# Kernel tuning notes

Measured on AMD Instinct MI355X. Metric: run time of the kernel, lower is better.

Reference implementation:

```python
import jax, jax.numpy as jnp
import numpy as np

REG = 0.1  # config['reg']


def _poly_filter(s, gammas):
    # Horner evaluation of sum_k gammas[k] * s**k (monomial basis, depth K=len-1).
    out = jnp.full_like(s, gammas[-1])
    for k in range(gammas.shape[0] - 2, -1, -1):
        out = out * s + gammas[k]
    return out


def setup_inputs() -> dict:
    key = jax.random.key(0)
    k1, k2, k3, k4, k5 = jax.random.split(key, 5)
    B, H, N, R = 4, 8, 4096, 64
    U = jax.random.normal(k1, (B, H, N, R), dtype=jnp.float32)
    Sigma = jax.random.normal(k2, (B, H, 1, R), dtype=jnp.float32)
    svd_V = jax.random.normal(k3, (B, H, N, R), dtype=jnp.float32)
    V = jax.random.normal(k4, (B, H, N, R), dtype=jnp.float32)
    mask = jnp.ones((B, N), dtype=jnp.float32)
    # learnable polynomial coefficients; gamma_0 fixed to 1 (fixI=True)
    gammas = jnp.concatenate([jnp.ones((1,), jnp.float32),
                              0.1 * jax.random.normal(k5, (4,), dtype=jnp.float32)])
    return {"U": U, "Sigma": Sigma, "svd_V": svd_V, "V": V, "mask": mask, "gammas": gammas}


def reference(U, Sigma, svd_V, V, mask, gammas):
    # Q: softmax over rank dim r
    Q = jax.nn.softmax(U, axis=-1)                                      # [B,H,N,r]
    # K: masked softmax over sequence dim N
    Kmat = jax.nn.softmax(svd_V - 1e9 * (1.0 - mask[:, None, :, None]), axis=-2)
    S = jax.nn.sigmoid(Sigma)                                           # [B,H,1,r]
    graph_filter = _poly_filter(S, gammas)                              # [B,H,1,r]
    # linear-attention ordering: (Q*filt) @ (K^T @ V), never forms NxN
    KtV = jnp.einsum('bhnr,bhnd->bhrd', Kmat, V)                        # [B,H,r,d]
    X = jnp.einsum('bhnr,bhrd->bhnd', Q * graph_filter, KtV)            # [B,H,N,d]
    r = Q.shape[-1]
    eye = jnp.eye(r, dtype=Q.dtype)
    symQ = jnp.einsum('bhnr,bhns->bhrs', Q, Q) - eye
    ortho_loss = REG * jnp.mean(jnp.abs(symQ), axis=(1, 2, 3))
    symK = jnp.einsum('bhnr,bhns->bhrs', Kmat, Kmat) - eye
    ortho_loss = ortho_loss + REG * jnp.mean(jnp.abs(symK), axis=(1, 2, 3))
    return X, ortho_loss
```

## Files before the change

### kernel.cpp

```cpp
#include <hip/hip_runtime.h>
#include <math.h>

#define NB 4
#define NH 8
#define BHN 32
#define SN 4096
#define RR 64
#define REGC 0.1f

#define MCH 16
#define MROWS 256
#define XCH 32
#define XROWS 128

typedef short s16x8 __attribute__((ext_vector_type(8)));
typedef float f32x4 __attribute__((ext_vector_type(4)));

__device__ __forceinline__ float wave_sum(float v) {
    #pragma unroll
    for (int off = 32; off; off >>= 1) v += __shfl_xor(v, off, 64);
    return v;
}
__device__ __forceinline__ float wave_sum64(float v) {
    v += __int_as_float(__builtin_amdgcn_update_dpp(0, __float_as_int(v), 0x121, 0xf, 0xf, true));
    v += __int_as_float(__builtin_amdgcn_update_dpp(0, __float_as_int(v), 0x122, 0xf, 0xf, true));
    v += __int_as_float(__builtin_amdgcn_update_dpp(0, __float_as_int(v), 0x124, 0xf, 0xf, true));
    v += __int_as_float(__builtin_amdgcn_update_dpp(0, __float_as_int(v), 0x128, 0xf, 0xf, true));
    v += __shfl_xor(v, 16, 64);
    v += __shfl_xor(v, 32, 64);
    return v;
}
__device__ __forceinline__ float octet_sum(float v) {
    v += __int_as_float(__builtin_amdgcn_update_dpp(0, __float_as_int(v), 0xB1, 0xf, 0xf, true));
    v += __int_as_float(__builtin_amdgcn_update_dpp(0, __float_as_int(v), 0x4E, 0xf, 0xf, true));
    v += __shfl_xor(v, 4, 64);
    return v;
}
__device__ __forceinline__ unsigned short f2bf(float x) {
    unsigned int u = __float_as_uint(x);
    u += 0x7FFFu + ((u >> 16) & 1u);
    return (unsigned short)(u >> 16);
}
__device__ __forceinline__ float bf2f(unsigned short h) {
    return __uint_as_float(((unsigned int)h) << 16);
}
__device__ __forceinline__ unsigned int packbf(float a, float b) {
    return (unsigned int)f2bf(a) | ((unsigned int)f2bf(b) << 16);
}
__device__ __forceinline__ s16x8 ldfrag(const unsigned int* p) {
    uint4 r = *(const uint4*)p;
    return __builtin_bit_cast(s16x8, r);
}
__device__ __forceinline__ int swz(int row, int blk) {
    return (row << 5) + (((blk ^ (row & 7))) << 2);
}
__device__ __forceinline__ uint4 pack8(const float* x) {
    return make_uint4(packbf(x[0], x[1]), packbf(x[2], x[3]),
                      packbf(x[4], x[5]), packbf(x[6], x[7]));
}

__global__ void k_zero_loss(float* loss) {
    if (threadIdx.x < NB) loss[threadIdx.x] = 0.0f;
}

#define PH 0
#define VH 2048
#define QH 4096
__launch_bounds__(512, 4)
__global__ void k_main(const float* __restrict__ U, const float* __restrict__ sv,
                       const float* __restrict__ V, const float* __restrict__ mask,
                       float* __restrict__ ktv_part, float* __restrict__ symk_part,
                       float* __restrict__ symq_part, float* __restrict__ colsum_part) {
    __shared__ __align__(16) unsigned int sm[12288];
    const int chunk = blockIdx.x, bh = blockIdx.y, b = bh >> 3;
    const int t = threadIdx.x, l = t & 63, w = t >> 6;
    const int r15 = l & 15, quad = l >> 4;
    const int ni = w & 3, mi0 = (w >> 2) << 1;
    const size_t rowbase = (size_t)bh * SN * RR;
    const int row0 = chunk * MROWS;

    float csum = 0.0f;
    f32x4 aKV[2], aSK[2], aSQ[2];
    #pragma unroll
    for (int j = 0; j < 2; j++) {
        aKV[j] = (f32x4){0.f, 0.f, 0.f, 0.f};
        aSK[j] = (f32x4){0.f, 0.f, 0.f, 0.f};
        aSQ[j] = (f32x4){0.f, 0.f, 0.f, 0.f};
    }

    float bu[2][8], bx[2][8], bv[2][8];
    #pragma unroll
    for (int i = 0; i < 8; i++) {
        const size_t off = rowbase + (size_t)(row0 + 8 * w + i) * RR + l;
        bu[0][i] = U[off]; bx[0][i] = sv[off]; bv[0][i] = V[off];
    }

    #pragma unroll
    for (int s = 0; s < 4; s++) {
        const int cur = s & 1, nxt = cur ^ 1;
        const int nb = row0 + s * 64;
        const int bufb = cur * 6144;
        float bm[8];
        #pragma unroll
        for (int i = 0; i < 8; i++) bm[i] = mask[b * SN + nb + 8 * w + i];
        float q[8], p[8];
        #pragma unroll
        for (int i = 0; i < 8; i++) {
            const float eu = __expf(bu[cur][i]);
            q[i] = eu * (1.0f / wave_sum64(eu));
        }
        #pragma unroll
        for (int i = 0; i < 8; i++) {
            p[i] = __expf(bx[cur][i] - 1e9f * (1.0f - bm[i]));
            csum += p[i];
        }
        if (s < 3) {
            #pragma unroll
            for (int i = 0; i < 8; i++) {
                const size_t off = rowbase + (size_t)(nb + 64 + 8 * w + i) * RR + l;
                bu[nxt][i] = U[off]; bx[nxt][i] = sv[off]; bv[nxt][i] = V[off];
            }
        }
        const uint4 ph = pack8(p);
        const uint4 vh = pack8(bv[cur]);
        const uint4 qh = pack8(q);
        const int wbase = bufb + (l << 5) + ((w ^ (l & 7)) << 2);
        *(uint4*)(sm + PH + wbase) = ph;
        *(uint4*)(sm + VH + wbase) = vh;
        *(uint4*)(sm + QH + wbase) = qh;
        __syncthreads();
        #pragma unroll
        for (int ks = 0; ks < 2; ks++) {
            const int ub = ks * 4 + quad;
            s16x8 Ah[2], AQ[2];
            #pragma unroll
            for (int j = 0; j < 2; j++) {
                const int oa = bufb + swz((mi0 + j) * 16 + r15, ub);
                Ah[j] = ldfrag(sm + PH + oa);
                AQ[j] = ldfrag(sm + QH + oa);
            }
            const int ob = bufb + swz(ni * 16 + r15, ub);
            const s16x8 Bvh = ldfrag(sm + VH + ob);
            const s16x8 Bph = ldfrag(sm + PH + ob);
            const s16x8 Bq  = ldfrag(sm + QH + ob);
            #pragma unroll
            for (int j = 0; j < 2; j++) {
                aKV[j] = __builtin_amdgcn_mfma_f32_16x16x32_bf16(Ah[j], Bvh, aKV[j], 0, 0, 0);
                aSK[j] = __builtin_amdgcn_mfma_f32_16x16x32_bf16(Ah[j], Bph, aSK[j], 0, 0, 0);
                aSQ[j] = __builtin_amdgcn_mfma_f32_16x16x32_bf16(AQ[j], Bq,  aSQ[j], 0, 0, 0);
            }
        }
    }
    const size_t pb = ((size_t)bh * MCH + chunk) * 4096;
    #pragma unroll
    for (int j = 0; j < 2; j++)
        #pragma unroll
        for (int r = 0; r < 4; r++) {
            const int e = ((mi0 + j) * 16 + quad * 4 + r) * 64 + ni * 16 + r15;
            ktv_part[pb + e]  = aKV[j][r];
            symk_part[pb + e] = aSK[j][r];
            symq_part[pb + e] = aSQ[j][r];
        }
    __syncthreads();
    float* smf = (float*)sm;
    smf[w * 64 + l] = csum;
    __syncthreads();
    if (w == 0) {
        float scol = 0.f;
        #pragma unroll
        for (int j = 0; j < 8; j++) scol += smf[j * 64 + l];
        colsum_part[(bh * MCH + chunk) * 64 + l] = scol;
    }
}

__global__ void k_finalize(const float* __restrict__ ktv_part, const float* __restrict__ symk_part,
                           const float* __restrict__ symq_part, const float* __restrict__ colsum_part,
                           const float* __restrict__ Sigma, const float* __restrict__ gammas,
                           unsigned short* __restrict__ ktvt_hi, unsigned short* __restrict__ ktvt_lo,
                           float* __restrict__ loss) {
    const int rb = blockIdx.x, bh = blockIdx.y, b = bh >> 3, t = threadIdx.x;
    __shared__ float cs[64];
    if (t < 64) {
        float s = 0.f;
        for (int c = 0; c < MCH; c++) s += colsum_part[(bh * MCH + c) * 64 + t];
        cs[t] = s;
    }
    __syncthreads();
    const float g0 = gammas[0], g1 = gammas[1], g2 = gammas[2], g3 = gammas[3], g4 = gammas[4];
    float lsum = 0.0f;
    #pragma unroll
    for (int o = 0; o < 2; o++) {
        const int idx = rb * 512 + o * 256 + t;
        const int r = idx >> 6, c = idx & 63;
        float kv = 0.f, sk = 0.f, sq = 0.f;
        for (int ch = 0; ch < MCH; ch++) {
            const size_t pb = ((size_t)bh * MCH + ch) * 4096 + idx;
            kv += ktv_part[pb]; sk += symk_part[pb]; sq += symq_part[pb];
        }
        const float iSr = 1.0f / cs[r], iSc = 1.0f / cs[c];
        kv *= iSr;
        sk *= iSr * iSc;
        const float sg = 1.0f / (1.0f + __expf(-Sigma[bh * 64 + r]));
        float f = g4; f = f * sg + g3; f = f * sg + g2; f = f * sg + g1; f = f * sg + g0;
        const float kvf = kv * f;
        const unsigned short h = f2bf(kvf);
        ktvt_hi[bh * 4096 + c * 64 + r] = h;
        ktvt_lo[bh * 4096 + c * 64 + r] = f2bf(kvf - bf2f(h));
        const float eye = (r == c) ? 1.0f : 0.0f;
        lsum += fabsf(sk - eye) + fabsf(sq - eye);
    }
    lsum = wave_sum(lsum);
    __shared__ float smr[4];
    if ((t & 63) == 0) smr[t >> 6] = lsum;
    __syncthreads();
    if (t == 0)
        atomicAdd(loss + b, (REGC / (NH * 64.0f * 64.0f)) * (smr[0] + smr[1] + smr[2] + smr[3]));
}

__launch_bounds__(512, 8)
__global__ void k_xq(const float* __restrict__ U,
                     const unsigned short* __restrict__ ktvt_hi,
                     const unsigned short* __restrict__ ktvt_lo,
                     float* __restrict__ Xout) {
    __shared__ __align__(16) unsigned int sm[4096];
    const int chunk = blockIdx.x, bh = blockIdx.y;
    const int t = threadIdx.x, l = t & 63, w = t >> 6;
    const int r15 = l & 15, quad = l >> 4;
    const int ni = w & 3, mi0 = (w >> 2) << 1;
    const size_t rowbase = (size_t)bh * SN * RR;
    const int row0 = chunk * XROWS;
    const int nl = 8 * w + (l >> 3);
    const int c0 = (l & 7) * 8;

    s16x8 Bh[2], Bl[2];
    #pragma unroll
    for (int ks = 0; ks < 2; ks++) {
        const int idx = (ni * 16 + r15) * 64 + ks * 32 + quad * 8;
        Bh[ks] = __builtin_bit_cast(s16x8, *(const uint4*)(ktvt_hi + (size_t)bh * 4096 + idx));
        Bl[ks] = __builtin_bit_cast(s16x8, *(const uint4*)(ktvt_lo + (size_t)bh * 4096 + idx));
    }

    float4 ba[2], bb[2];
    {
        const float* src = U + rowbase + (size_t)(row0 + nl) * RR + c0;
        ba[0] = *(const float4*)src;
        bb[0] = *(const float4*)(src + 4);
    }

    #pragma unroll
    for (int s = 0; s < 2; s++) {
        const int cur = s & 1, nxt = cur ^ 1;
        const int nb = row0 + s * 64;
        const int bufb = cur * 2048;
        float e[8];
        e[0] = __expf(ba[cur].x); e[1] = __expf(ba[cur].y);
        e[2] = __expf(ba[cur].z); e[3] = __expf(ba[cur].w);
        e[4] = __expf(bb[cur].x); e[5] = __expf(bb[cur].y);
        e[6] = __expf(bb[cur].z); e[7] = __expf(bb[cur].w);
        float loc = 0.f;
        #pragma unroll
        for (int i = 0; i < 8; i++) loc += e[i];
        const float inv = 1.0f / octet_sum(loc);
        if (s < 1) {
            const float* src = U + rowbase + (size_t)(nb + 64 + nl) * RR + c0;
            ba[nxt] = *(const float4*)src;
            bb[nxt] = *(const float4*)(src + 4);
        }
        float q[8];
        #pragma unroll
        for (int i = 0; i < 8; i++) q[i] = e[i] * inv;
        *(uint4*)(sm + bufb + swz(nl, l & 7)) = pack8(q);
        __syncthreads();
        f32x4 acc[2];
        acc[0] = (f32x4){0.f, 0.f, 0.f, 0.f};
        acc[1] = (f32x4){0.f, 0.f, 0.f, 0.f};
        #pragma unroll
        for (int ks = 0; ks < 2; ks++) {
            #pragma unroll
            for (int jj = 0; jj < 2; jj++) {
                const int oa = bufb + swz((mi0 + jj) * 16 + r15, ks * 4 + quad);
                const s16x8 Ah = ldfrag(sm + oa);
                acc[jj] = __builtin_amdgcn_mfma_f32_16x16x32_bf16(Ah, Bh[ks], acc[jj], 0, 0, 0);
                acc[jj] = __builtin_amdgcn_mfma_f32_16x16x32_bf16(Ah, Bl[ks], acc[jj], 0, 0, 0);
            }
        }
        #pragma unroll
        for (int jj = 0; jj < 2; jj++)
            #pragma unroll
            for (int r = 0; r < 4; r++) {
                const int n = nb + (mi0 + jj) * 16 + quad * 4 + r;
                Xout[rowbase + (size_t)n * RR + ni * 16 + r15] = acc[jj][r];
            }
    }
}

extern "C" void kernel_launch(void* const* d_in, const int* in_sizes, int n_in,
                              void* d_out, int out_size, void* d_ws, size_t ws_size,
                              hipStream_t stream) {
    (void)in_sizes; (void)n_in; (void)out_size; (void)ws_size;
    const float* U      = (const float*)d_in[0];
    const float* Sigma  = (const float*)d_in[1];
    const float* sv     = (const float*)d_in[2];
    const float* V      = (const float*)d_in[3];
    const float* mask   = (const float*)d_in[4];
    const float* gammas = (const float*)d_in[5];

    float* X    = (float*)d_out;
    float* loss = X + (size_t)BHN * SN * RR;

    float* ws          = (float*)d_ws;
    float* ktv_part    = ws;
    float* symk_part   = ktv_part + (size_t)BHN * MCH * 4096;
    float* symq_part   = symk_part + (size_t)BHN * MCH * 4096;
    float* colsum_part = symq_part + (size_t)BHN * MCH * 4096;
    unsigned short* ktvt_hi = (unsigned short*)(colsum_part + BHN * MCH * 64);
    unsigned short* ktvt_lo = ktvt_hi + BHN * 4096;

    hipLaunchKernelGGL(k_zero_loss, dim3(1), dim3(64), 0, stream, loss);
    hipLaunchKernelGGL(k_main, dim3(MCH, BHN), dim3(512), 0, stream,
                       U, sv, V, mask, ktv_part, symk_part, symq_part, colsum_part);
    hipLaunchKernelGGL(k_finalize, dim3(8, BHN), dim3(256), 0, stream,
                       ktv_part, symk_part, symq_part, colsum_part, Sigma, gammas,
                       ktvt_hi, ktvt_lo, loss);
    hipLaunchKernelGGL(k_xq, dim3(XCH, BHN), dim3(512), 0, stream,
                       U, ktvt_hi, ktvt_lo, X);
}
```

Before: 157.7 us.

## Split main pass into more chunks, drop loss-zero kernel, vectorize finalize

Doubles the number of chunks in the main reduction kernel (128 rows each, single LDS buffer, higher occupancy bound) to give more blocks in flight. Removes the separate loss-zeroing launch and atomics by writing per-block loss partials and reducing them inside the X kernel. Vectorizes the finalize partial-sum reads with float2, uses a raw hardware reciprocal instead of division, and moves prefetch loads earlier. This doubles the partial-buffer traffic read in finalize and relies on the approximate rcp for accuracy.

```diff
diff --git a/kernel.cpp b/kernel.cpp
--- a/kernel.cpp
+++ b/kernel.cpp
@@ -8,8 +8,8 @@
 #define RR 64
 #define REGC 0.1f
 
-#define MCH 16
-#define MROWS 256
+#define MCH 32
+#define MROWS 128
 #define XCH 32
 #define XROWS 128
 
@@ -36,6 +36,9 @@
     v += __shfl_xor(v, 4, 64);
     return v;
 }
+__device__ __forceinline__ float fastrcp(float x) {
+    float r; asm("v_rcp_f32 %0, %1" : "=v"(r) : "v"(x)); return r;
+}
 __device__ __forceinline__ unsigned short f2bf(float x) {
     unsigned int u = __float_as_uint(x);
     u += 0x7FFFu + ((u >> 16) & 1u);
@@ -59,19 +62,15 @@
                       packbf(x[4], x[5]), packbf(x[6], x[7]));
 }
 
-__global__ void k_zero_loss(float* loss) {
-    if (threadIdx.x < NB) loss[threadIdx.x] = 0.0f;
-}
-
 #define PH 0
 #define VH 2048
 #define QH 4096
-__launch_bounds__(512, 4)
+__launch_bounds__(512, 8)
 __global__ void k_main(const float* __restrict__ U, const float* __restrict__ sv,
                        const float* __restrict__ V, const float* __restrict__ mask,
                        float* __restrict__ ktv_part, float* __restrict__ symk_part,
                        float* __restrict__ symq_part, float* __restrict__ colsum_part) {
-    __shared__ __align__(16) unsigned int sm[12288];
+    __shared__ __align__(16) unsigned int sm[6144];
     const int chunk = blockIdx.x, bh = blockIdx.y, b = bh >> 3;
     const int t = threadIdx.x, l = t & 63, w = t >> 6;
     const int r15 = l & 15, quad = l >> 4;
@@ -96,10 +95,16 @@
     }
 
     #pragma unroll
-    for (int s = 0; s < 4; s++) {
+    for (int s = 0; s < 2; s++) {
         const int cur = s & 1, nxt = cur ^ 1;
         const int nb = row0 + s * 64;
-        const int bufb = cur * 6144;
+        if (s < 1) {
+            #pragma unroll
+            for (int i = 0; i < 8; i++) {
+                const size_t off = rowbase + (size_t)(nb + 64 + 8 * w + i) * RR + l;
+                bu[nxt][i] = U[off]; bx[nxt][i] = sv[off]; bv[nxt][i] = V[off];
+            }
+        }
         float bm[8];
         #pragma unroll
         for (int i = 0; i < 8; i++) bm[i] = mask[b * SN + nb + 8 * w + i];
@@ -107,24 +112,18 @@
         #pragma unroll
         for (int i = 0; i < 8; i++) {
             const float eu = __expf(bu[cur][i]);
-            q[i] = eu * (1.0f / wave_sum64(eu));
+            q[i] = eu * fastrcp(wave_sum64(eu));
         }
         #pragma unroll
         for (int i = 0; i < 8; i++) {
             p[i] = __expf(bx[cur][i] - 1e9f * (1.0f - bm[i]));
             csum += p[i];
         }
-        if (s < 3) {
-            #pragma unroll
-            for (int i = 0; i < 8; i++) {
-                const size_t off = rowbase + (size_t)(nb + 64 + 8 * w + i) * RR + l;
-                bu[nxt][i] = U[off]; bx[nxt][i] = sv[off]; bv[nxt][i] = V[off];
-            }
-        }
         const uint4 ph = pack8(p);
         const uint4 vh = pack8(bv[cur]);
         const uint4 qh = pack8(q);
-        const int wbase = bufb + (l << 5) + ((w ^ (l & 7)) << 2);
+        const int wbase = (l << 5) + ((w ^ (l & 7)) << 2);
+        if (s > 0) __syncthreads();
         *(uint4*)(sm + PH + wbase) = ph;
         *(uint4*)(sm + VH + wbase) = vh;
         *(uint4*)(sm + QH + wbase) = qh;
@@ -135,11 +134,11 @@
             s16x8 Ah[2], AQ[2];
             #pragma unroll
             for (int j = 0; j < 2; j++) {
-                const int oa = bufb + swz((mi0 + j) * 16 + r15, ub);
+                const int oa = swz((mi0 + j) * 16 + r15, ub);
                 Ah[j] = ldfrag(sm + PH + oa);
                 AQ[j] = ldfrag(sm + QH + oa);
             }
-            const int ob = bufb + swz(ni * 16 + r15, ub);
+            const int ob = swz(ni * 16 + r15, ub);
             const s16x8 Bvh = ldfrag(sm + VH + ob);
             const s16x8 Bph = ldfrag(sm + PH + ob);
             const s16x8 Bq  = ldfrag(sm + QH + ob);
@@ -177,8 +176,8 @@
                            const float* __restrict__ symq_part, const float* __restrict__ colsum_part,
                            const float* __restrict__ Sigma, const float* __restrict__ gammas,
                            unsigned short* __restrict__ ktvt_hi, unsigned short* __restrict__ ktvt_lo,
-                           float* __restrict__ loss) {
-    const int rb = blockIdx.x, bh = blockIdx.y, b = bh >> 3, t = threadIdx.x;
+                           float* __restrict__ loss_part) {
+    const int rb = blockIdx.x, bh = blockIdx.y, t = threadIdx.x;
     __shared__ float cs[64];
     if (t < 64) {
         float s = 0.f;
@@ -187,41 +186,45 @@
     }
     __syncthreads();
     const float g0 = gammas[0], g1 = gammas[1], g2 = gammas[2], g3 = gammas[3], g4 = gammas[4];
-    float lsum = 0.0f;
-    #pragma unroll
-    for (int o = 0; o < 2; o++) {
-        const int idx = rb * 512 + o * 256 + t;
-        const int r = idx >> 6, c = idx & 63;
-        float kv = 0.f, sk = 0.f, sq = 0.f;
-        for (int ch = 0; ch < MCH; ch++) {
-            const size_t pb = ((size_t)bh * MCH + ch) * 4096 + idx;
-            kv += ktv_part[pb]; sk += symk_part[pb]; sq += symq_part[pb];
-        }
-        const float iSr = 1.0f / cs[r], iSc = 1.0f / cs[c];
-        kv *= iSr;
-        sk *= iSr * iSc;
-        const float sg = 1.0f / (1.0f + __expf(-Sigma[bh * 64 + r]));
-        float f = g4; f = f * sg + g3; f = f * sg + g2; f = f * sg + g1; f = f * sg + g0;
-        const float kvf = kv * f;
-        const unsigned short h = f2bf(kvf);
-        ktvt_hi[bh * 4096 + c * 64 + r] = h;
-        ktvt_lo[bh * 4096 + c * 64 + r] = f2bf(kvf - bf2f(h));
-        const float eye = (r == c) ? 1.0f : 0.0f;
-        lsum += fabsf(sk - eye) + fabsf(sq - eye);
-    }
+    const int idx = rb * 512 + t * 2;
+    const int r = idx >> 6, c = idx & 63;
+    float2 kv = make_float2(0.f, 0.f), sk = make_float2(0.f, 0.f), sq = make_float2(0.f, 0.f);
+    #pragma unroll 4
+    for (int ch = 0; ch < MCH; ch++) {
+        const size_t pb = ((size_t)bh * MCH + ch) * 4096 + idx;
+        const float2 a = *(const float2*)(ktv_part + pb);
+        const float2 bq = *(const float2*)(symk_part + pb);
+        const float2 cq = *(const float2*)(symq_part + pb);
+        kv.x += a.x;  kv.y += a.y;
+        sk.x += bq.x; sk.y += bq.y;
+        sq.x += cq.x; sq.y += cq.y;
+    }
+    const float iSr = fastrcp(cs[r]);
+    const float iSc0 = fastrcp(cs[c]), iSc1 = fastrcp(cs[c + 1]);
+    const float sg = fastrcp(1.0f + __expf(-Sigma[bh * 64 + r]));
+    float f = g4; f = f * sg + g3; f = f * sg + g2; f = f * sg + g1; f = f * sg + g0;
+    const float kvf0 = kv.x * iSr * f, kvf1 = kv.y * iSr * f;
+    const unsigned short h0 = f2bf(kvf0), h1 = f2bf(kvf1);
+    ktvt_hi[bh * 4096 + c * 64 + r] = h0;
+    ktvt_lo[bh * 4096 + c * 64 + r] = f2bf(kvf0 - bf2f(h0));
+    ktvt_hi[bh * 4096 + (c + 1) * 64 + r] = h1;
+    ktvt_lo[bh * 4096 + (c + 1) * 64 + r] = f2bf(kvf1 - bf2f(h1));
+    const float eye0 = (r == c) ? 1.0f : 0.0f, eye1 = (r == c + 1) ? 1.0f : 0.0f;
+    float lsum = fabsf(sk.x * iSr * iSc0 - eye0) + fabsf(sk.y * iSr * iSc1 - eye1)
+               + fabsf(sq.x - eye0) + fabsf(sq.y - eye1);
     lsum = wave_sum(lsum);
     __shared__ float smr[4];
     if ((t & 63) == 0) smr[t >> 6] = lsum;
     __syncthreads();
-    if (t == 0)
-        atomicAdd(loss + b, (REGC / (NH * 64.0f * 64.0f)) * (smr[0] + smr[1] + smr[2] + smr[3]));
+    if (t == 0) loss_part[bh * 8 + rb] = smr[0] + smr[1] + smr[2] + smr[3];
 }
 
 __launch_bounds__(512, 8)
 __global__ void k_xq(const float* __restrict__ U,
                      const unsigned short* __restrict__ ktvt_hi,
                      const unsigned short* __restrict__ ktvt_lo,
-                     float* __restrict__ Xout) {
+                     const float* __restrict__ loss_part,
+                     float* __restrict__ Xout, float* __restrict__ loss) {
     __shared__ __align__(16) unsigned int sm[4096];
     const int chunk = blockIdx.x, bh = blockIdx.y;
     const int t = threadIdx.x, l = t & 63, w = t >> 6;
@@ -232,6 +235,11 @@
     const int nl = 8 * w + (l >> 3);
     const int c0 = (l & 7) * 8;
 
+    if (chunk == 0 && bh == 0 && t < 256) {
+        const float v = wave_sum(loss_part[t]);
+        if ((t & 63) == 0) loss[t >> 6] = (REGC / (NH * 64.0f * 64.0f)) * v;
+    }
+
     s16x8 Bh[2], Bl[2];
     #pragma unroll
     for (int ks = 0; ks < 2; ks++) {
@@ -252,6 +260,11 @@
         const int cur = s & 1, nxt = cur ^ 1;
         const int nb = row0 + s * 64;
         const int bufb = cur * 2048;
+        if (s < 1) {
+            const float* src = U + rowbase + (size_t)(nb + 64 + nl) * RR + c0;
+            ba[nxt] = *(const float4*)src;
+            bb[nxt] = *(const float4*)(src + 4);
+        }
         float e[8];
         e[0] = __expf(ba[cur].x); e[1] = __expf(ba[cur].y);
         e[2] = __expf(ba[cur].z); e[3] = __expf(ba[cur].w);
@@ -260,12 +273,7 @@
         float loc = 0.f;
         #pragma unroll
         for (int i = 0; i < 8; i++) loc += e[i];
-        const float inv = 1.0f / octet_sum(loc);
-        if (s < 1) {
-            const float* src = U + rowbase + (size_t)(nb + 64 + nl) * RR + c0;
-            ba[nxt] = *(const float4*)src;
-            bb[nxt] = *(const float4*)(src + 4);
-        }
+        const float inv = fastrcp(octet_sum(loc));
         float q[8];
         #pragma unroll
         for (int i = 0; i < 8; i++) q[i] = e[i] * inv;
@@ -313,15 +321,15 @@
     float* symk_part   = ktv_part + (size_t)BHN * MCH * 4096;
     float* symq_part   = symk_part + (size_t)BHN * MCH * 4096;
     float* colsum_part = symq_part + (size_t)BHN * MCH * 4096;
-    unsigned short* ktvt_hi = (unsigned short*)(colsum_part + BHN * MCH * 64);
+    float* loss_part   = colsum_part + BHN * MCH * 64;
+    unsigned short* ktvt_hi = (unsigned short*)(loss_part + 256);
     unsigned short* ktvt_lo = ktvt_hi + BHN * 4096;
 
-    hipLaunchKernelGGL(k_zero_loss, dim3(1), dim3(64), 0, stream, loss);
     hipLaunchKernelGGL(k_main, dim3(MCH, BHN), dim3(512), 0, stream,
                        U, sv, V, mask, ktv_part, symk_part, symq_part, colsum_part);
     hipLaunchKernelGGL(k_finalize, dim3(8, BHN), dim3(256), 0, stream,
                        ktv_part, symk_part, symq_part, colsum_part, Sigma, gammas,
-                       ktvt_hi, ktvt_lo, loss);
+                       ktvt_hi, ktvt_lo, loss_part);
     hipLaunchKernelGGL(k_xq, dim3(XCH, BHN), dim3(512), 0, stream,
-                       U, ktvt_hi, ktvt_lo, X);
-}
+                       U, ktvt_hi, ktvt_lo, loss_part, X, loss);
+}
```

After: 188.1 us. 1.19x slower.
